# Optimization experiments

Hardware: AMD Instinct MI355X
Metric: run time of the kernel (lower is better)

## Reference

```python
import jax, jax.numpy as jnp
import numpy as np


def setup_inputs() -> dict:
    key = jax.random.key(0)
    ks = jax.random.split(key, 5)
    B, T, C, es = 32, 2048, 256, 256
    stdv = 1.0 / np.sqrt(es)
    return {
        "x": jax.random.normal(ks[0], (B, T, C), dtype=jnp.float32),
        "h0": jnp.zeros((B, es), dtype=jnp.float32),
        "c0": jnp.zeros((B, es), dtype=jnp.float32),
        "W1": jax.random.uniform(ks[1], (C, 4 * es), minval=-stdv, maxval=stdv, dtype=jnp.float32),
        "W2": jax.random.uniform(ks[2], (es, 4 * es), minval=-stdv, maxval=stdv, dtype=jnp.float32),
        "b1": jax.random.uniform(ks[3], (4 * es,), minval=-stdv, maxval=stdv, dtype=jnp.float32),
        "b2": jax.random.uniform(ks[4], (4 * es,), minval=-stdv, maxval=stdv, dtype=jnp.float32),
    }


def reference(x, h0, c0, W1, W2, b1, b2):
    B, T, C = x.shape
    es = W2.shape[0]
    # input-side gate preactivations for all timesteps at once: [T, B, 4*es]
    pre = jnp.transpose(jnp.einsum("btc,cg->btg", x, W1) + b1 + b2, (1, 0, 2))

    def step(carry, pre_t):
        h, c = carry
        v = pre_t + h @ W2  # [B, 4*es]
        f = jax.nn.sigmoid(v[:, :es])
        i = jax.nn.sigmoid(v[:, es:2 * es])
        o = jax.nn.sigmoid(v[:, 2 * es:3 * es])
        c_hat = jnp.tanh(v[:, 3 * es:])
        c_new = f * c + i * c_hat
        h_new = o * jnp.tanh(c_new)
        return (h_new, c_new), h_new

    (h, c), out_h_2 = jax.lax.scan(step, (h0, c0), pre)  # out_h_2: [T, B, es]
    # torch.cat(out_h, dim=-1): [B, T*es]
    out_h_1 = jnp.transpose(out_h_2, (1, 0, 2)).reshape(B, T * es)
    return (out_h_1, out_h_2, (h, c))
```

## Files before the change

### kernel.cpp

```cpp
#include <hip/hip_runtime.h>

typedef unsigned int u32;
typedef unsigned short u16;
typedef __attribute__((ext_vector_type(2))) _Float16 h2v;
typedef __attribute__((ext_vector_type(4))) _Float16 f16x4;
typedef __attribute__((ext_vector_type(4))) float f32x4;

#define BB 32
#define TT 2048
#define CC 256
#define ESZ 256
#define GG 1024

#define RREG 100
#define NCH 7

__device__ __forceinline__ float fdot2u(u32 a, u32 b, float c) {
#if __has_builtin(__builtin_amdgcn_fdot2)
  return __builtin_amdgcn_fdot2(__builtin_bit_cast(h2v, a), __builtin_bit_cast(h2v, b), c, false);
#else
  h2v av = __builtin_bit_cast(h2v, a), bv = __builtin_bit_cast(h2v, b);
  return c + (float)av[0] * (float)bv[0] + (float)av[1] * (float)bv[1];
#endif
}

__device__ __forceinline__ float sigm_f(float x) {
  float e = __builtin_amdgcn_exp2f(x * -1.442695041f);
  return __builtin_amdgcn_rcpf(1.0f + e);
}
__device__ __forceinline__ float tanh_f(float x) {
  float e = __builtin_amdgcn_exp2f(x * 2.885390082f);
  return 1.0f - 2.0f * __builtin_amdgcn_rcpf(e + 1.0f);
}

__global__ void k_pack_w2(const float* __restrict__ W2, u32* __restrict__ W2p) {
  int gid = blockIdx.x * 256 + threadIdx.x;
  int m = gid >> 10, j = gid & 1023;
  _Float16 lo = (_Float16)W2[(size_t)(2 * m) * GG + j];
  _Float16 hi = (_Float16)W2[(size_t)(2 * m + 1) * GG + j];
  W2p[gid] = (u32)__builtin_bit_cast(u16, lo) | ((u32)__builtin_bit_cast(u16, hi) << 16);
}

__global__ __launch_bounds__(256, 2) void k_pre_gemm(
    const float* __restrict__ x, const float* __restrict__ W1,
    const float* __restrict__ b1, const float* __restrict__ b2,
    _Float16* __restrict__ pre) {
  __shared__ __attribute__((aligned(16))) _Float16 Al[128 * 36];
  __shared__ __attribute__((aligned(16))) _Float16 Bl[64 * 36];
  const int tid = threadIdx.x;
  const int lane = tid & 63, wv = tid >> 6;
  const int wr = wv >> 1, wc = wv & 1;
  const int rowBase = blockIdx.x * 128;
  const int colBase = blockIdx.y * 64;

  f32x4 acc[4][2];
#pragma unroll
  for (int mi = 0; mi < 4; ++mi)
#pragma unroll
    for (int ni = 0; ni < 2; ++ni) acc[mi][ni] = (f32x4){0.f, 0.f, 0.f, 0.f};

  for (int k0 = 0; k0 < 256; k0 += 32) {
#pragma unroll
    for (int i = 0; i < 4; ++i) {
      int fidx = tid + 256 * i;
      int row = fidx >> 3, kc = (fidx & 7) * 4;
      const float4 v = *(const float4*)(x + (size_t)(rowBase + row) * 256 + k0 + kc);
      f16x4 hv = { (_Float16)v.x, (_Float16)v.y, (_Float16)v.z, (_Float16)v.w };
      *(f16x4*)&Al[row * 36 + kc] = hv;
    }
#pragma unroll
    for (int i = 0; i < 8; ++i) {
      int idx = tid + 256 * i;
      int k = idx >> 6, n = idx & 63;
      Bl[n * 36 + k] = (_Float16)W1[(size_t)(k0 + k) * GG + colBase + n];
    }
    __syncthreads();

#pragma unroll
    for (int kk = 0; kk < 2; ++kk) {
      int ka = (lane >> 4) * 4 + kk * 16;
      f16x4 af[4], bf[2];
#pragma unroll
      for (int mi = 0; mi < 4; ++mi)
        af[mi] = *(const f16x4*)&Al[(wr * 64 + mi * 16 + (lane & 15)) * 36 + ka];
#pragma unroll
      for (int ni = 0; ni < 2; ++ni)
        bf[ni] = *(const f16x4*)&Bl[(wc * 32 + ni * 16 + (lane & 15)) * 36 + ka];
#pragma unroll
      for (int mi = 0; mi < 4; ++mi)
#pragma unroll
        for (int ni = 0; ni < 2; ++ni)
          acc[mi][ni] = __builtin_amdgcn_mfma_f32_16x16x16f16(af[mi], bf[ni], acc[mi][ni], 0, 0, 0);
    }
    __syncthreads();
  }

#pragma unroll
  for (int ni = 0; ni < 2; ++ni) {
    int col = colBase + wc * 32 + ni * 16 + (lane & 15);
    float bias = b1[col] + b2[col];
#pragma unroll
    for (int mi = 0; mi < 4; ++mi) {
      int r0 = rowBase + wr * 64 + mi * 16 + (lane >> 4) * 4;
#pragma unroll
      for (int rr = 0; rr < 4; ++rr)
        pre[(size_t)(r0 + rr) * GG + col] = (_Float16)(acc[mi][ni][rr] + bias);
    }
  }
}

__global__ __launch_bounds__(512, 2) void k_lstm_rec(
    const _Float16* __restrict__ pre, const u32* __restrict__ W2p,
    const float* __restrict__ h0, const float* __restrict__ c0,
    float* __restrict__ out1, float* __restrict__ out2,
    float* __restrict__ hN, float* __restrict__ cN) {
  extern __shared__ __attribute__((aligned(16))) char smem[];
  uint4* W2Lw = (uint4*)smem;
  const uint4* W2L = (const uint4*)smem;
  _Float16* hbuf = (_Float16*)(smem + NCH * 1024 * 16);
  const u32* hrow = (const u32*)(smem + NCH * 1024 * 16);
  float2* exch = (float2*)(smem + NCH * 1024 * 16 + 512);

  const int t = threadIdx.x;
  const int b = blockIdx.x;
  const int j = t & 255, half = t >> 8;
  const int lane = t & 63;
  const int col0 = j + half * 512;
  const int col1 = col0 + 256;

  u32 wA[RREG], wB[RREG];
#pragma unroll
  for (int m = 0; m < RREG; ++m) {
    wA[m] = W2p[m * GG + col0];
    wB[m] = W2p[m * GG + col1];
  }
  for (int idx = t; idx < NCH * 1024; idx += 512) {
    int cch = idx >> 10, col = idx & 1023;
    int m0 = RREG + 4 * cch;
    uint4 v;
    v.x = W2p[(m0 + 0) * GG + col];
    v.y = W2p[(m0 + 1) * GG + col];
    v.z = W2p[(m0 + 2) * GG + col];
    v.w = W2p[(m0 + 3) * GG + col];
    W2Lw[idx] = v;
  }

  float creg = 0.f, hlast = 0.f;
  if (!half) {
    hbuf[j] = (_Float16)h0[b * ESZ + j];
    creg = c0[b * ESZ + j];
  }
  __syncthreads();

  const _Float16* preB = pre + (size_t)b * TT * GG;
  const size_t o1base = (size_t)b * TT * ESZ + j;

  _Float16 q0 = preB[col0], q1 = preB[col1];

  for (int s = 0; s < TT; ++s) {
    u32 hv0 = hrow[lane];
    u32 hv1 = hrow[64 + lane];

    float a0 = (float)q0, a1 = (float)q1;
    if (s + 1 < TT) {
      const _Float16* pn = preB + (size_t)(s + 1) * GG;
      q0 = pn[col0];
      q1 = pn[col1];
    }
    float p0 = 0.f, p1 = 0.f;

#pragma unroll
    for (int m = 0; m < 64; ++m) {
      u32 hm = (u32)__builtin_amdgcn_readlane((int)hv0, m);
      a0 = fdot2u(hm, wA[m], a0);
      a1 = fdot2u(hm, wB[m], a1);
    }
#pragma unroll
    for (int m = 0; m < RREG - 64; ++m) {
      u32 hm = (u32)__builtin_amdgcn_readlane((int)hv1, m);
      p0 = fdot2u(hm, wA[64 + m], p0);
      p1 = fdot2u(hm, wB[64 + m], p1);
    }
#pragma unroll
    for (int cch = 0; cch < NCH; ++cch) {
      uint4 wa = W2L[cch * 1024 + col0];
      uint4 wb = W2L[cch * 1024 + col1];
      u32 h0m = (u32)__builtin_amdgcn_readlane((int)hv1, RREG - 64 + 4 * cch + 0);
      u32 h1m = (u32)__builtin_amdgcn_readlane((int)hv1, RREG - 64 + 4 * cch + 1);
      u32 h2m = (u32)__builtin_amdgcn_readlane((int)hv1, RREG - 64 + 4 * cch + 2);
      u32 h3m = (u32)__builtin_amdgcn_readlane((int)hv1, RREG - 64 + 4 * cch + 3);
      p0 = fdot2u(h0m, wa.x, p0); p1 = fdot2u(h0m, wb.x, p1);
      p0 = fdot2u(h1m, wa.y, p0); p1 = fdot2u(h1m, wb.y, p1);
      p0 = fdot2u(h2m, wa.z, p0); p1 = fdot2u(h2m, wb.z, p1);
      p0 = fdot2u(h3m, wa.w, p0); p1 = fdot2u(h3m, wb.w, p1);
    }
    a0 += p0;
    a1 += p1;

    float fg = 0.f, ig = 0.f;
    if (half) {
      exch[j] = make_float2(sigm_f(a0), tanh_f(a1));
    } else {
      fg = sigm_f(a0);
      ig = sigm_f(a1);
    }
    __syncthreads();

    if (!half) {
      float2 e = exch[j];
      creg = fg * creg + ig * e.y;
      float hv = e.x * tanh_f(creg);
      hlast = hv;
      out1[o1base + (size_t)s * ESZ] = hv;
      out2[(size_t)s * (BB * ESZ) + b * ESZ + j] = hv;
      hbuf[j] = (_Float16)hv;
    }
    __syncthreads();
  }

  if (!half) {
    hN[b * ESZ + j] = hlast;
    cN[b * ESZ + j] = creg;
  }
}

extern "C" void kernel_launch(void* const* d_in, const int* in_sizes, int n_in,
                              void* d_out, int out_size, void* d_ws, size_t ws_size,
                              hipStream_t stream) {
  const float* x  = (const float*)d_in[0];
  const float* h0 = (const float*)d_in[1];
  const float* c0 = (const float*)d_in[2];
  const float* W1 = (const float*)d_in[3];
  const float* W2 = (const float*)d_in[4];
  const float* b1 = (const float*)d_in[5];
  const float* b2 = (const float*)d_in[6];

  float* out1 = (float*)d_out;
  float* out2 = out1 + (size_t)BB * TT * ESZ;
  float* hN   = out2 + (size_t)BB * TT * ESZ;
  float* cN   = hN + BB * ESZ;

  _Float16* pre = (_Float16*)d_ws;
  u32* W2p = (u32*)((char*)d_ws + (size_t)BB * TT * GG * 2);

  k_pack_w2<<<512, 256, 0, stream>>>(W2, W2p);
  k_pre_gemm<<<dim3(512, 16), 256, 0, stream>>>(x, W1, b1, b2, pre);

  const int ldsBytes = NCH * 1024 * 16 + 512 + 2048;
  hipFuncSetAttribute((const void*)k_lstm_rec, hipFuncAttributeMaxDynamicSharedMemorySize, ldsBytes);
  k_lstm_rec<<<BB, 512, ldsBytes, stream>>>(pre, W2p, h0, c0, out1, out2, hN, cN);
}
```

Baseline: 3.737 ms.

## Split W2 across registers, LDS, and per-step global streaming in recurrence

Fewer W2 rows now stay in registers per thread (80 instead of 100) and in LDS (6 chunks instead of 7). The remaining 24 packed rows are read from a new pre-packed global buffer at every timestep, presumably out of L2, and their loads are issued early in the step. The gate exchange changes so both halves compute their activations symmetrically and write four separate float planes, and the kernel uses waves_per_eu and asm register pinning. This is meant to ease register pressure and spills, at the cost of extra global/L2 traffic on the serial critical path every step.

After: 5.231 ms. 1.4x slower.

```diff
diff --git a/kernel.cpp b/kernel.cpp
--- a/kernel.cpp
+++ b/kernel.cpp
@@ -12,8 +12,9 @@
 #define ESZ 256
 #define GG 1024
 
-#define RREG 100
-#define NCH 7
+#define MREG 80
+#define NLDS 6
+#define NSTR 6
 
 __device__ __forceinline__ float fdot2u(u32 a, u32 b, float c) {
 #if __has_builtin(__builtin_amdgcn_fdot2)
@@ -39,6 +40,18 @@
   _Float16 lo = (_Float16)W2[(size_t)(2 * m) * GG + j];
   _Float16 hi = (_Float16)W2[(size_t)(2 * m + 1) * GG + j];
   W2p[gid] = (u32)__builtin_bit_cast(u16, lo) | ((u32)__builtin_bit_cast(u16, hi) << 16);
+}
+
+__global__ void k_pack_stream(const u32* __restrict__ W2p, uint4* __restrict__ W2s) {
+  int idx = blockIdx.x * 256 + threadIdx.x;
+  int c = idx >> 10, col = idx & 1023;
+  int m0 = (MREG + NLDS * 4) + 4 * c;
+  uint4 v;
+  v.x = W2p[(m0 + 0) * GG + col];
+  v.y = W2p[(m0 + 1) * GG + col];
+  v.z = W2p[(m0 + 2) * GG + col];
+  v.w = W2p[(m0 + 3) * GG + col];
+  W2s[idx] = v;
 }
 
 __global__ __launch_bounds__(256, 2) void k_pre_gemm(
@@ -109,17 +122,20 @@
   }
 }
 
-__global__ __launch_bounds__(512, 2) void k_lstm_rec(
+__global__ __launch_bounds__(512)
+__attribute__((amdgpu_waves_per_eu(2, 2)))
+void k_lstm_rec(
     const _Float16* __restrict__ pre, const u32* __restrict__ W2p,
+    const uint4* __restrict__ W2s,
     const float* __restrict__ h0, const float* __restrict__ c0,
     float* __restrict__ out1, float* __restrict__ out2,
     float* __restrict__ hN, float* __restrict__ cN) {
   extern __shared__ __attribute__((aligned(16))) char smem[];
   uint4* W2Lw = (uint4*)smem;
   const uint4* W2L = (const uint4*)smem;
-  _Float16* hbuf = (_Float16*)(smem + NCH * 1024 * 16);
-  const u32* hrow = (const u32*)(smem + NCH * 1024 * 16);
-  float2* exch = (float2*)(smem + NCH * 1024 * 16 + 512);
+  _Float16* hbuf = (_Float16*)(smem + NLDS * 1024 * 16);
+  const u32* hrow = (const u32*)(smem + NLDS * 1024 * 16);
+  float* exch = (float*)(smem + NLDS * 1024 * 16 + 512);
 
   const int t = threadIdx.x;
   const int b = blockIdx.x;
@@ -128,15 +144,18 @@
   const int col0 = j + half * 512;
   const int col1 = col0 + 256;
 
-  u32 wA[RREG], wB[RREG];
-#pragma unroll
-  for (int m = 0; m < RREG; ++m) {
+  u32 wA[MREG], wB[MREG];
+#pragma unroll
+  for (int m = 0; m < MREG; ++m) {
     wA[m] = W2p[m * GG + col0];
     wB[m] = W2p[m * GG + col1];
   }
-  for (int idx = t; idx < NCH * 1024; idx += 512) {
-    int cch = idx >> 10, col = idx & 1023;
-    int m0 = RREG + 4 * cch;
+#pragma unroll
+  for (int m = 0; m < MREG; ++m) asm volatile("" : "+v"(wA[m]), "+v"(wB[m]));
+
+  for (int idx = t; idx < NLDS * 1024; idx += 512) {
+    int c = idx >> 10, col = idx & 1023;
+    int m0 = MREG + 4 * c;
     uint4 v;
     v.x = W2p[(m0 + 0) * GG + col];
     v.y = W2p[(m0 + 1) * GG + col];
@@ -153,13 +172,18 @@
   __syncthreads();
 
   const _Float16* preB = pre + (size_t)b * TT * GG;
-  const size_t o1base = (size_t)b * TT * ESZ + j;
-
   _Float16 q0 = preB[col0], q1 = preB[col1];
 
   for (int s = 0; s < TT; ++s) {
     u32 hv0 = hrow[lane];
     u32 hv1 = hrow[64 + lane];
+
+    uint4 sA[NSTR], sB[NSTR];
+#pragma unroll
+    for (int i = 0; i < NSTR; ++i) {
+      sA[i] = W2s[i * 1024 + col0];
+      sB[i] = W2s[i * 1024 + col1];
+    }
 
     float a0 = (float)q0, a1 = (float)q1;
     if (s + 1 < TT) {
@@ -176,42 +200,53 @@
       a1 = fdot2u(hm, wB[m], a1);
     }
 #pragma unroll
-    for (int m = 0; m < RREG - 64; ++m) {
-      u32 hm = (u32)__builtin_amdgcn_readlane((int)hv1, m);
-      p0 = fdot2u(hm, wA[64 + m], p0);
-      p1 = fdot2u(hm, wB[64 + m], p1);
-    }
-#pragma unroll
-    for (int cch = 0; cch < NCH; ++cch) {
-      uint4 wa = W2L[cch * 1024 + col0];
-      uint4 wb = W2L[cch * 1024 + col1];
-      u32 h0m = (u32)__builtin_amdgcn_readlane((int)hv1, RREG - 64 + 4 * cch + 0);
-      u32 h1m = (u32)__builtin_amdgcn_readlane((int)hv1, RREG - 64 + 4 * cch + 1);
-      u32 h2m = (u32)__builtin_amdgcn_readlane((int)hv1, RREG - 64 + 4 * cch + 2);
-      u32 h3m = (u32)__builtin_amdgcn_readlane((int)hv1, RREG - 64 + 4 * cch + 3);
-      p0 = fdot2u(h0m, wa.x, p0); p1 = fdot2u(h0m, wb.x, p1);
-      p0 = fdot2u(h1m, wa.y, p0); p1 = fdot2u(h1m, wb.y, p1);
-      p0 = fdot2u(h2m, wa.z, p0); p1 = fdot2u(h2m, wb.z, p1);
-      p0 = fdot2u(h3m, wa.w, p0); p1 = fdot2u(h3m, wb.w, p1);
+    for (int i = 0; i < MREG - 64; ++i) {
+      u32 hm = (u32)__builtin_amdgcn_readlane((int)hv1, i);
+      p0 = fdot2u(hm, wA[64 + i], p0);
+      p1 = fdot2u(hm, wB[64 + i], p1);
+    }
+#pragma unroll
+    for (int c = 0; c < NLDS; ++c) {
+      uint4 la = W2L[c * 1024 + col0];
+      uint4 lb = W2L[c * 1024 + col1];
+      u32 lax[4] = {la.x, la.y, la.z, la.w};
+      u32 lbx[4] = {lb.x, lb.y, lb.z, lb.w};
+#pragma unroll
+      for (int r = 0; r < 4; ++r) {
+        u32 hm = (u32)__builtin_amdgcn_readlane((int)hv1, (MREG - 64) + 4 * c + r);
+        p0 = fdot2u(hm, lax[r], p0);
+        p1 = fdot2u(hm, lbx[r], p1);
+      }
+    }
+#pragma unroll
+    for (int c = 0; c < NSTR; ++c) {
+      u32 sax[4] = {sA[c].x, sA[c].y, sA[c].z, sA[c].w};
+      u32 sbx[4] = {sB[c].x, sB[c].y, sB[c].z, sB[c].w};
+#pragma unroll
+      for (int r = 0; r < 4; ++r) {
+        u32 hm = (u32)__builtin_amdgcn_readlane((int)hv1, (MREG - 64) + NLDS * 4 + 4 * c + r);
+        a0 = fdot2u(hm, sax[r], a0);
+        a1 = fdot2u(hm, sbx[r], a1);
+      }
     }
     a0 += p0;
     a1 += p1;
 
-    float fg = 0.f, ig = 0.f;
-    if (half) {
-      exch[j] = make_float2(sigm_f(a0), tanh_f(a1));
-    } else {
-      fg = sigm_f(a0);
-      ig = sigm_f(a1);
-    }
+    float g0 = sigm_f(a0);
+    float g1 = half ? tanh_f(a1) : sigm_f(a1);
+    exch[(half * 2 + 0) * 260 + j] = g0;
+    exch[(half * 2 + 1) * 260 + j] = g1;
     __syncthreads();
 
     if (!half) {
-      float2 e = exch[j];
-      creg = fg * creg + ig * e.y;
-      float hv = e.x * tanh_f(creg);
+      float fg = exch[0 * 260 + j];
+      float ig = exch[1 * 260 + j];
+      float og = exch[2 * 260 + j];
+      float ch = exch[3 * 260 + j];
+      creg = fg * creg + ig * ch;
+      float hv = og * tanh_f(creg);
       hlast = hv;
-      out1[o1base + (size_t)s * ESZ] = hv;
+      out1[(size_t)b * TT * ESZ + (size_t)s * ESZ + j] = hv;
       out2[(size_t)s * (BB * ESZ) + b * ESZ + j] = hv;
       hbuf[j] = (_Float16)hv;
     }
@@ -242,11 +277,13 @@
 
   _Float16* pre = (_Float16*)d_ws;
   u32* W2p = (u32*)((char*)d_ws + (size_t)BB * TT * GG * 2);
+  uint4* W2s = (uint4*)((char*)W2p + 128 * GG * 4);
 
   k_pack_w2<<<512, 256, 0, stream>>>(W2, W2p);
+  k_pack_stream<<<NSTR * 4, 256, 0, stream>>>(W2p, W2s);
   k_pre_gemm<<<dim3(512, 16), 256, 0, stream>>>(x, W1, b1, b2, pre);
 
-  const int ldsBytes = NCH * 1024 * 16 + 512 + 2048;
+  const int ldsBytes = NLDS * 1024 * 16 + 512 + 4 * 260 * 4;
   hipFuncSetAttribute((const void*)k_lstm_rec, hipFuncAttributeMaxDynamicSharedMemorySize, ldsBytes);
-  k_lstm_rec<<<BB, 512, ldsBytes, stream>>>(pre, W2p, h0, c0, out1, out2, hN, cN);
-}
+  k_lstm_rec<<<BB, 512, ldsBytes, stream>>>(pre, W2p, W2s, h0, c0, out1, out2, hN, cN);
+}
```
